# Optimization experiments

Hardware: AMD Instinct MI355X
Metric: run time of the kernel (lower is better)

## Reference

```python
import jax, jax.numpy as jnp
import numpy as np
from jax import lax

# --- tree geometry (matches init_kwargs) ---
B_CHAIN = 16384      # backbone length (generation-0 scan path, excluding root)
S_SIDE = 15          # side-chain length per backbone atom (generation-1 scans)
NATM = 1 + B_CHAIN + B_CHAIN * S_SIDE   # 262145, node 0 is the virtual root
N_SEL_PER = 4        # masked DOFs per non-root node (phi_p, theta, d, phi_c)


def _rx(a):
    c, s = jnp.cos(a), jnp.sin(a)
    z, o = jnp.zeros_like(a), jnp.ones_like(a)
    return jnp.stack([jnp.stack([o, z, z, z], -1),
                      jnp.stack([z, c, -s, z], -1),
                      jnp.stack([z, s, c, z], -1),
                      jnp.stack([z, z, z, o], -1)], -2)


def _ry(a):
    c, s = jnp.cos(a), jnp.sin(a)
    z, o = jnp.zeros_like(a), jnp.ones_like(a)
    return jnp.stack([jnp.stack([c, z, s, z], -1),
                      jnp.stack([z, o, z, z], -1),
                      jnp.stack([-s, z, c, z], -1),
                      jnp.stack([z, z, z, o], -1)], -2)


def _rz(a):
    c, s = jnp.cos(a), jnp.sin(a)
    z, o = jnp.zeros_like(a), jnp.ones_like(a)
    return jnp.stack([jnp.stack([c, -s, z, z], -1),
                      jnp.stack([s, c, z, z], -1),
                      jnp.stack([z, z, o, z], -1),
                      jnp.stack([z, z, z, o], -1)], -2)


def _t(x, y, z):
    zz, o = jnp.zeros_like(x), jnp.ones_like(x)
    return jnp.stack([jnp.stack([o, zz, zz, x], -1),
                      jnp.stack([zz, o, zz, y], -1),
                      jnp.stack([zz, zz, o, z], -1),
                      jnp.stack([zz, zz, zz, o], -1)], -2)


def _mm(a, b):
    return jnp.einsum('...ij,...jk->...ik', a, b)


def setup_inputs() -> dict:
    key = jax.random.key(0)
    k_dofs, = jax.random.split(key, 1)
    rng = np.random.default_rng(0)

    # DOF mask: the 4 bond DOFs of every non-root node (selected_dofs)
    node_idx = np.repeat(np.arange(1, NATM, dtype=np.int32), N_SEL_PER)
    dof_idx = np.tile(np.arange(N_SEL_PER, dtype=np.int32), NATM - 1)

    # doftype: 0=root, 1=jump (first backbone node), 2=bond
    doftype = np.full(NATM, 2, dtype=np.int32)
    doftype[0] = 0
    doftype[1] = 1

    # generation-0 scan: root + backbone chain (parent[i] = i-1)
    gen0_nodes = np.arange(B_CHAIN + 1, dtype=np.int32)
    # generation-1 scans: one side-chain path per backbone node
    gen1_nodes = np.arange(1 + B_CHAIN, NATM, dtype=np.int32).reshape(B_CHAIN, S_SIDE)
    gen1_parents = np.arange(1, B_CHAIN + 1, dtype=np.int32)  # parent of each scan's first node

    # kintree.id: id[0] = -1 (root unused), id[1:] a permutation of system indices
    kin_id = np.empty(NATM, dtype=np.int32)
    kin_id[0] = -1
    kin_id[1:] = rng.permutation(NATM - 1).astype(np.int32)

    dofs = 0.5 * jax.random.normal(k_dofs, (N_SEL_PER * (NATM - 1),), dtype=jnp.float32)
    full_dofs = jnp.zeros((NATM, 9), dtype=jnp.float32)

    return {
        'dofs': dofs,
        'full_dofs': full_dofs,
        'node_idx': jnp.asarray(node_idx),
        'dof_idx': jnp.asarray(dof_idx),
        'doftype': jnp.asarray(doftype),
        'gen0_nodes': jnp.asarray(gen0_nodes),
        'gen1_nodes': jnp.asarray(gen1_nodes),
        'gen1_parents': jnp.asarray(gen1_parents),
        'kin_id': jnp.asarray(kin_id),
    }


def reference(dofs, full_dofs, node_idx, dof_idx, doftype, gen0_nodes,
              gen1_nodes, gen1_parents, kin_id):
    natm = full_dofs.shape[0]

    # --- DOFMaskingFunc: scatter selected dofs into the background dofs ---
    full = full_dofs.at[node_idx, dof_idx].set(dofs)

    # --- per-node local homogeneous transforms from dofs ---
    # bond: Rx(phi_p) . Rz(theta) . Tx(d) . Rx(phi_c)
    zero = jnp.zeros_like(full[:, 0])
    ht_bond = _mm(_mm(_rx(full[:, 0]), _rz(full[:, 1])),
                  _mm(_t(full[:, 2], zero, zero), _rx(full[:, 3])))
    # jump: T(x,y,z) . Rz(g) . Ry(b) . Rx(a)
    ht_jump = _mm(_t(full[:, 0], full[:, 1], full[:, 2]),
                  _mm(_rz(full[:, 5]), _mm(_ry(full[:, 4]), _rx(full[:, 3]))))
    dt = doftype[:, None, None]
    eye = jnp.broadcast_to(jnp.eye(4, dtype=full.dtype), (natm, 4, 4))
    ht = jnp.where(dt == 2, ht_bond, jnp.where(dt == 1, ht_jump, eye))

    # --- generation-ordered forward-kinematics scan ---
    # gen 0: single long path starting at root; global[k] = M0 @ ... @ Mk
    g0 = lax.associative_scan(_mm, ht[gen0_nodes], axis=0)
    ht_global = jnp.zeros((natm, 4, 4), dtype=full.dtype).at[gen0_nodes].set(g0)

    # gen 1: independent paths; seed each with its parent's global transform
    ms = ht[gen1_nodes]                                   # [n_scans, S, 4, 4]
    ms = ms.at[:, 0].set(_mm(ht_global[gen1_parents], ms[:, 0]))
    g1 = lax.associative_scan(_mm, ms, axis=1)
    ht_global = ht_global.at[gen1_nodes.reshape(-1)].set(g1.reshape(-1, 4, 4))

    kincoords = ht_global[:, :3, 3]                       # [natm, 3]

    # --- KinematicOperation: scatter kin coords into system coords by id ---
    coords = jnp.full((natm - 1, 3), jnp.nan, dtype=kincoords.dtype)
    coords = coords.at[kin_id[1:]].set(kincoords[1:])
    return coords[None, ...]
```

## Files before the change

kernel.cpp:

```cpp
#include <hip/hip_runtime.h>
#include <math.h>


#define B_CHAIN 16384
#define S_SIDE 15
#define NATM (1 + B_CHAIN + B_CHAIN * S_SIDE)
#define NB (B_CHAIN + 1)
#define NODES_PER_LANE 8
#define LANES 64
#define NODES_PER_CHUNK (NODES_PER_LANE * LANES)
#define CHUNK_SHIFT 9
#define NCHUNK ((NB + NODES_PER_CHUNK - 1) / NODES_PER_CHUNK)

struct Aff { float m[12]; };

__device__ __forceinline__ Aff aff_id() {
    Aff a;
    a.m[0]=1.f; a.m[1]=0.f; a.m[2]=0.f;  a.m[3]=0.f;
    a.m[4]=0.f; a.m[5]=1.f; a.m[6]=0.f;  a.m[7]=0.f;
    a.m[8]=0.f; a.m[9]=0.f; a.m[10]=1.f; a.m[11]=0.f;
    return a;
}

__device__ __forceinline__ Aff aff_mul(const Aff& A, const Aff& B) {
    Aff C;
#pragma unroll
    for (int r = 0; r < 3; ++r) {
        const float a0 = A.m[r*4+0], a1 = A.m[r*4+1], a2 = A.m[r*4+2];
#pragma unroll
        for (int c = 0; c < 3; ++c)
            C.m[r*4+c] = a0*B.m[0*4+c] + a1*B.m[1*4+c] + a2*B.m[2*4+c];
        C.m[r*4+3] = a0*B.m[3] + a1*B.m[7] + a2*B.m[11] + A.m[r*4+3];
    }
    return C;
}

__device__ __forceinline__ Aff bond_ht(float a, float b, float x, float cang) {
    float sa, ca, sb, cb, sc, cc;
    sincosf(a, &sa, &ca);
    sincosf(b, &sb, &cb);
    sincosf(cang, &sc, &cc);
    Aff M;
    M.m[0] = cb;      M.m[1] = -sb*cc;           M.m[2] = sb*sc;            M.m[3]  = cb*x;
    M.m[4] = ca*sb;   M.m[5] = ca*cb*cc - sa*sc; M.m[6] = -ca*cb*sc - sa*cc;M.m[7]  = ca*sb*x;
    M.m[8] = sa*sb;   M.m[9] = sa*cb*cc + ca*sc; M.m[10]= -sa*cb*sc + ca*cc;M.m[11] = sa*sb*x;
    return M;
}

__device__ __forceinline__ Aff node_ht(int n, const float* __restrict__ dofs) {
    if (n == 0) return aff_id();
    const float4 d = *reinterpret_cast<const float4*>(dofs + 4*(n-1));
    if (n == 1) {
        float s, c; sincosf(d.w, &s, &c);
        Aff M = aff_id();
        M.m[3] = d.x; M.m[7] = d.y; M.m[11] = d.z;
        M.m[5] = c; M.m[6] = -s; M.m[9] = s; M.m[10] = c;
        return M;
    }
    return bond_ht(d.x, d.y, d.z, d.w);
}

__device__ __forceinline__ Aff aff_shfl_up(const Aff& v, int delta) {
    Aff r;
#pragma unroll
    for (int i = 0; i < 12; ++i) r.m[i] = __shfl_up(v.m[i], delta, 64);
    return r;
}

__device__ __forceinline__ void aff_store(float* p, const Aff& f) {
    float4* q = reinterpret_cast<float4*>(p);
    q[0] = make_float4(f.m[0], f.m[1], f.m[2],  f.m[3]);
    q[1] = make_float4(f.m[4], f.m[5], f.m[6],  f.m[7]);
    q[2] = make_float4(f.m[8], f.m[9], f.m[10], f.m[11]);
}

__device__ __forceinline__ Aff aff_load(const float* p) {
    const float4* q = reinterpret_cast<const float4*>(p);
    float4 r0 = q[0], r1 = q[1], r2 = q[2];
    Aff f;
    f.m[0]=r0.x; f.m[1]=r0.y; f.m[2]=r0.z;  f.m[3]=r0.w;
    f.m[4]=r1.x; f.m[5]=r1.y; f.m[6]=r1.z;  f.m[7]=r1.w;
    f.m[8]=r2.x; f.m[9]=r2.y; f.m[10]=r2.z; f.m[11]=r2.w;
    return f;
}

__global__ __launch_bounds__(64) void k_scan_local(const float* __restrict__ dofs,
                                                   float* __restrict__ gbuf,
                                                   float* __restrict__ totals) {
    const int lane = threadIdx.x;
    const int chunk = blockIdx.x;
    const int base = chunk * NODES_PER_CHUNK + lane * NODES_PER_LANE;

    Aff pref[NODES_PER_LANE];
    Aff acc;
#pragma unroll
    for (int j = 0; j < NODES_PER_LANE; ++j) {
        const int n = base + j;
        Aff m = (n < NB) ? node_ht(n, dofs) : aff_id();
        acc = (j == 0) ? m : aff_mul(acc, m);
        pref[j] = acc;
    }

    Aff incl = acc;
#pragma unroll
    for (int s = 1; s < 64; s <<= 1) {
        Aff up = aff_shfl_up(incl, s);
        if (lane >= s) incl = aff_mul(up, incl);
    }
    Aff excl = aff_shfl_up(incl, 1);
    const bool have_excl = (lane > 0);

#pragma unroll
    for (int j = 0; j < NODES_PER_LANE; ++j) {
        const int n = base + j;
        if (n < NB) {
            Aff f = have_excl ? aff_mul(excl, pref[j]) : pref[j];
            aff_store(gbuf + n * 12, f);
        }
    }
    if (lane == 63) aff_store(totals + chunk * 12, incl);
}

__global__ __launch_bounds__(64) void k_scan_totals(float* __restrict__ totals) {
    const int lane = threadIdx.x;
    Aff v = (lane < NCHUNK) ? aff_load(totals + lane * 12) : aff_id();
#pragma unroll
    for (int s = 1; s < 64; s <<= 1) {
        Aff up = aff_shfl_up(v, s);
        if (lane >= s) v = aff_mul(up, v);
    }
    if (lane < NCHUNK) aff_store(totals + lane * 12, v);
}

__global__ __launch_bounds__(64) void k_finalize(const float* __restrict__ dofs,
                                                 const int* __restrict__ kin_id,
                                                 const float* __restrict__ gbuf,
                                                 const float* __restrict__ totals,
                                                 float* __restrict__ out) {
    const int c = blockIdx.x * 64 + threadIdx.x;
    if (c >= B_CHAIN) return;
    const int p = c + 1;

    Aff G = aff_load(gbuf + p * 12);
    const int chunk = p >> CHUNK_SHIFT;
    if (chunk > 0) G = aff_mul(aff_load(totals + (chunk - 1) * 12), G);

    int kid = kin_id[p];
    out[3*kid+0] = G.m[3]; out[3*kid+1] = G.m[7]; out[3*kid+2] = G.m[11];

    const int atom0 = 1 + B_CHAIN + c * S_SIDE;
#pragma unroll
    for (int s = 0; s < S_SIDE; ++s) {
        const int atom = atom0 + s;
        const float4 d = *reinterpret_cast<const float4*>(dofs + 4*(atom-1));
        Aff M = bond_ht(d.x, d.y, d.z, d.w);
        G = aff_mul(G, M);
        kid = kin_id[atom];
        out[3*kid+0] = G.m[3]; out[3*kid+1] = G.m[7]; out[3*kid+2] = G.m[11];
    }
}

extern "C" void kernel_launch(void* const* d_in, const int* in_sizes, int n_in,
                              void* d_out, int out_size, void* d_ws, size_t ws_size,
                              hipStream_t stream) {
    const float* dofs   = (const float*)d_in[0];
    const int*   kin_id = (const int*)  d_in[8];
    float* ws = (float*)d_ws;
    float* gbuf   = ws;
    float* totals = ws + NB * 12;

    k_scan_local <<<NCHUNK, 64, 0, stream>>>(dofs, gbuf, totals);
    k_scan_totals<<<1,      64, 0, stream>>>(totals);
    k_finalize   <<<(B_CHAIN + 63) / 64, 64, 0, stream>>>(dofs, kin_id, gbuf, totals,
                                                          (float*)d_out);
}
```

Before: 104.9 us.

## Parallelize side-chain scans across 16 lanes and fold totals scan into finalize

```diff
diff --git a/kernel.cpp b/kernel.cpp
--- a/kernel.cpp
+++ b/kernel.cpp
@@ -5,12 +5,9 @@
 #define B_CHAIN 16384
 #define S_SIDE 15
 #define NATM (1 + B_CHAIN + B_CHAIN * S_SIDE)
-#define NB (B_CHAIN + 1)
-#define NODES_PER_LANE 8
-#define LANES 64
-#define NODES_PER_CHUNK (NODES_PER_LANE * LANES)
-#define CHUNK_SHIFT 9
-#define NCHUNK ((NB + NODES_PER_CHUNK - 1) / NODES_PER_CHUNK)
+#define NODES_PER_LANE 4
+#define NODES_PER_CHUNK 256
+#define NCHUNK 64
 
 struct Aff { float m[12]; };
 
@@ -41,14 +38,13 @@
     sincosf(b, &sb, &cb);
     sincosf(cang, &sc, &cc);
     Aff M;
-    M.m[0] = cb;      M.m[1] = -sb*cc;           M.m[2] = sb*sc;            M.m[3]  = cb*x;
-    M.m[4] = ca*sb;   M.m[5] = ca*cb*cc - sa*sc; M.m[6] = -ca*cb*sc - sa*cc;M.m[7]  = ca*sb*x;
-    M.m[8] = sa*sb;   M.m[9] = sa*cb*cc + ca*sc; M.m[10]= -sa*cb*sc + ca*cc;M.m[11] = sa*sb*x;
+    M.m[0] = cb;      M.m[1] = -sb*cc;            M.m[2] = sb*sc;             M.m[3]  = cb*x;
+    M.m[4] = ca*sb;   M.m[5] = ca*cb*cc - sa*sc;  M.m[6] = -ca*cb*sc - sa*cc; M.m[7]  = ca*sb*x;
+    M.m[8] = sa*sb;   M.m[9] = sa*cb*cc + ca*sc;  M.m[10]= -sa*cb*sc + ca*cc; M.m[11] = sa*sb*x;
     return M;
 }
 
 __device__ __forceinline__ Aff node_ht(int n, const float* __restrict__ dofs) {
-    if (n == 0) return aff_id();
     const float4 d = *reinterpret_cast<const float4*>(dofs + 4*(n-1));
     if (n == 1) {
         float s, c; sincosf(d.w, &s, &c);
@@ -60,10 +56,10 @@
     return bond_ht(d.x, d.y, d.z, d.w);
 }
 
-__device__ __forceinline__ Aff aff_shfl_up(const Aff& v, int delta) {
+__device__ __forceinline__ Aff aff_shfl_up(const Aff& v, int delta, int width) {
     Aff r;
 #pragma unroll
-    for (int i = 0; i < 12; ++i) r.m[i] = __shfl_up(v.m[i], delta, 64);
+    for (int i = 0; i < 12; ++i) r.m[i] = __shfl_up(v.m[i], delta, width);
     return r;
 }
 
@@ -89,14 +85,13 @@
                                                    float* __restrict__ totals) {
     const int lane = threadIdx.x;
     const int chunk = blockIdx.x;
-    const int base = chunk * NODES_PER_CHUNK + lane * NODES_PER_LANE;
+    const int base = 1 + chunk * NODES_PER_CHUNK + lane * NODES_PER_LANE;
 
     Aff pref[NODES_PER_LANE];
     Aff acc;
 #pragma unroll
     for (int j = 0; j < NODES_PER_LANE; ++j) {
-        const int n = base + j;
-        Aff m = (n < NB) ? node_ht(n, dofs) : aff_id();
+        Aff m = node_ht(base + j, dofs);
         acc = (j == 0) ? m : aff_mul(acc, m);
         pref[j] = acc;
     }
@@ -104,60 +99,74 @@
     Aff incl = acc;
 #pragma unroll
     for (int s = 1; s < 64; s <<= 1) {
-        Aff up = aff_shfl_up(incl, s);
+        Aff up = aff_shfl_up(incl, s, 64);
         if (lane >= s) incl = aff_mul(up, incl);
     }
-    Aff excl = aff_shfl_up(incl, 1);
+    Aff excl = aff_shfl_up(incl, 1, 64);
     const bool have_excl = (lane > 0);
 
 #pragma unroll
     for (int j = 0; j < NODES_PER_LANE; ++j) {
-        const int n = base + j;
-        if (n < NB) {
-            Aff f = have_excl ? aff_mul(excl, pref[j]) : pref[j];
-            aff_store(gbuf + n * 12, f);
-        }
+        Aff f = have_excl ? aff_mul(excl, pref[j]) : pref[j];
+        aff_store(gbuf + (base + j - 1) * 12, f);
     }
     if (lane == 63) aff_store(totals + chunk * 12, incl);
 }
 
-__global__ __launch_bounds__(64) void k_scan_totals(float* __restrict__ totals) {
-    const int lane = threadIdx.x;
-    Aff v = (lane < NCHUNK) ? aff_load(totals + lane * 12) : aff_id();
+__global__ __launch_bounds__(256) void k_finalize(const float* __restrict__ dofs,
+                                                  const int* __restrict__ kin_id,
+                                                  const float* __restrict__ gbuf,
+                                                  const float* __restrict__ totals,
+                                                  float* __restrict__ out) {
+    __shared__ float s_tot[NCHUNK * 12];
+
+    if (threadIdx.x < 64) {
+        const int lane = threadIdx.x;
+        Aff v = aff_load(totals + lane * 12);
 #pragma unroll
-    for (int s = 1; s < 64; s <<= 1) {
-        Aff up = aff_shfl_up(v, s);
-        if (lane >= s) v = aff_mul(up, v);
+        for (int s = 1; s < 64; s <<= 1) {
+            Aff up = aff_shfl_up(v, s, 64);
+            if (lane >= s) v = aff_mul(up, v);
+        }
+#pragma unroll
+        for (int i = 0; i < 12; ++i) s_tot[lane * 12 + i] = v.m[i];
     }
-    if (lane < NCHUNK) aff_store(totals + lane * 12, v);
-}
+    __syncthreads();
 
-__global__ __launch_bounds__(64) void k_finalize(const float* __restrict__ dofs,
-                                                 const int* __restrict__ kin_id,
-                                                 const float* __restrict__ gbuf,
-                                                 const float* __restrict__ totals,
-                                                 float* __restrict__ out) {
-    const int c = blockIdx.x * 64 + threadIdx.x;
-    if (c >= B_CHAIN) return;
-    const int p = c + 1;
+    const int t = blockIdx.x * 256 + threadIdx.x;
+    const int c  = t >> 4;
+    const int ls = t & 15;
+    const int p  = c + 1;
 
-    Aff G = aff_load(gbuf + p * 12);
-    const int chunk = p >> CHUNK_SHIFT;
-    if (chunk > 0) G = aff_mul(aff_load(totals + (chunk - 1) * 12), G);
+    Aff V;
+    int idx;
+    if (ls == 0) {
+        V = aff_load(gbuf + (p - 1) * 12);
+        const int chunk = (p - 1) >> 8;
+        if (chunk > 0) {
+            Aff pre;
+#pragma unroll
+            for (int i = 0; i < 12; ++i) pre.m[i] = s_tot[(chunk - 1) * 12 + i];
+            V = aff_mul(pre, V);
+        }
+        idx = p;
+    } else {
+        const int atom = 1 + B_CHAIN + c * S_SIDE + (ls - 1);
+        const float4 d = *reinterpret_cast<const float4*>(dofs + 4*(atom-1));
+        V = bond_ht(d.x, d.y, d.z, d.w);
+        idx = atom;
+    }
 
-    int kid = kin_id[p];
-    out[3*kid+0] = G.m[3]; out[3*kid+1] = G.m[7]; out[3*kid+2] = G.m[11];
+#pragma unroll
+    for (int s = 1; s < 16; s <<= 1) {
+        Aff up = aff_shfl_up(V, s, 16);
+        if (ls >= s) V = aff_mul(up, V);
+    }
 
-    const int atom0 = 1 + B_CHAIN + c * S_SIDE;
-#pragma unroll
-    for (int s = 0; s < S_SIDE; ++s) {
-        const int atom = atom0 + s;
-        const float4 d = *reinterpret_cast<const float4*>(dofs + 4*(atom-1));
-        Aff M = bond_ht(d.x, d.y, d.z, d.w);
-        G = aff_mul(G, M);
-        kid = kin_id[atom];
-        out[3*kid+0] = G.m[3]; out[3*kid+1] = G.m[7]; out[3*kid+2] = G.m[11];
-    }
+    const int kid = kin_id[idx];
+    out[3*kid+0] = V.m[3];
+    out[3*kid+1] = V.m[7];
+    out[3*kid+2] = V.m[11];
 }
 
 extern "C" void kernel_launch(void* const* d_in, const int* in_sizes, int n_in,
@@ -167,10 +176,9 @@
     const int*   kin_id = (const int*)  d_in[8];
     float* ws = (float*)d_ws;
     float* gbuf   = ws;
-    float* totals = ws + NB * 12;
+    float* totals = ws + B_CHAIN * 12;
 
-    k_scan_local <<<NCHUNK, 64, 0, stream>>>(dofs, gbuf, totals);
-    k_scan_totals<<<1,      64, 0, stream>>>(totals);
-    k_finalize   <<<(B_CHAIN + 63) / 64, 64, 0, stream>>>(dofs, kin_id, gbuf, totals,
-                                                          (float*)d_out);
+    k_scan_local<<<NCHUNK, 64, 0, stream>>>(dofs, gbuf, totals);
+    k_finalize  <<<(B_CHAIN * 16) / 256, 256, 0, stream>>>(dofs, kin_id, gbuf, totals,
+                                                           (float*)d_out);
 }
```

After: 92.01 us. 12.3% less time.
